# Performance work log

Hardware: AMD Instinct MI355X
Metric: run time of the kernel (lower is better)

The kernel has to match this reference:

```python
import jax, jax.numpy as jnp
import numpy as np

N_HEADS = 8
D_HEAD = 16
D_IN = 128
N_NODES = 50000
N_EDGES = 600000


def setup_inputs() -> dict:
    key = jax.random.key(0)
    ks = jax.random.split(key, 7)
    x = jax.random.normal(ks[0], (N_NODES, D_IN), dtype=jnp.float32)
    edge_attr = jax.random.normal(ks[1], (N_EDGES, D_IN), dtype=jnp.float32)
    edge_index = jax.random.randint(ks[2], (2, N_EDGES), 0, N_NODES, dtype=jnp.int32)
    # Linear weights stored as [in, out] so projection is x @ W.
    s = 1.0 / np.sqrt(D_IN)
    WQ = jax.random.normal(ks[3], (D_IN, N_HEADS * D_HEAD), dtype=jnp.float32) * s
    WK = jax.random.normal(ks[4], (D_IN, N_HEADS * D_HEAD), dtype=jnp.float32) * s
    WV = jax.random.normal(ks[5], (D_IN, N_HEADS * D_HEAD), dtype=jnp.float32) * s
    WE = jax.random.normal(ks[6], (D_IN, N_HEADS * D_HEAD), dtype=jnp.float32) * s
    return {"x": x, "edge_attr": edge_attr, "edge_index": edge_index,
            "WQ": WQ, "WK": WK, "WV": WV, "WE": WE}


def reference(x, edge_attr, edge_index, WQ, WK, WV, WE):
    N = x.shape[0]
    q = (x @ WQ).reshape(N, N_HEADS, D_HEAD)
    k = (x @ WK).reshape(N, N_HEADS, D_HEAD)
    v = (x @ WV).reshape(N, N_HEADS, D_HEAD)
    e_proj = (edge_attr @ WE).reshape(-1, N_HEADS, D_HEAD)
    row, col = edge_index[0], edge_index[1]
    # per-edge gather-compute: [E, H, D]
    alpha = (k[row] * q[col]) * (1.0 / np.sqrt(D_HEAD))
    alpha = jnp.clip(alpha, -5.0, 5.0) * e_proj
    e_out = alpha  # update_edge_feats=True
    alphax = jnp.exp(jnp.clip(alpha.sum(-1, keepdims=True), -5.0, 5.0))  # [E, H, 1]
    wV = jax.ops.segment_sum(v[row] * alphax, col, num_segments=N)  # [N, H, D]
    z = jax.ops.segment_sum(alphax, col, num_segments=N)            # [N, H, 1]
    h_out = wV / (z + 1e-6)
    return h_out, e_out
```

## Files before the change

### kernel.cpp

```cpp
#include <hip/hip_runtime.h>

#define DIN 128
#define NHEADS 8
#define DHEAD 16
#define NPB 32
#define EPB 64

typedef __attribute__((ext_vector_type(8))) short short8;
typedef __attribute__((ext_vector_type(4))) float f32x4;

__device__ __forceinline__ float clip5(float x) {
    return fminf(fmaxf(x, -5.0f), 5.0f);
}

__device__ __forceinline__ unsigned short f2bf(float f) {
    unsigned u = __float_as_uint(f);
    unsigned r = (u + 0x7FFF + ((u >> 16) & 1)) >> 16;
    return (unsigned short)r;
}

__device__ __forceinline__ float b2f(unsigned short u) {
    return __uint_as_float((unsigned)u << 16);
}

__device__ __forceinline__ float bflo(unsigned u) {
    return __uint_as_float(u << 16);
}
__device__ __forceinline__ float bfhi(unsigned u) {
    return __uint_as_float(u & 0xffff0000u);
}


__device__ __forceinline__ void tile_gemm(const float xs[][DIN], int r0, int cg,
                                          const float* __restrict__ W,
                                          float4 acc[4]) {
#pragma unroll 4
    for (int kk = 0; kk < DIN; kk += 4) {
        float4 a[4];
#pragma unroll
        for (int i = 0; i < 4; ++i)
            a[i] = *(const float4*)&xs[r0 + i][kk];
#pragma unroll
        for (int t = 0; t < 4; ++t) {
            float4 w = *(const float4*)&W[(kk + t) * DIN + (cg << 2)];
#pragma unroll
            for (int i = 0; i < 4; ++i) {
                float av = ((const float*)&a[i])[t];
                acc[i].x = fmaf(av, w.x, acc[i].x);
                acc[i].y = fmaf(av, w.y, acc[i].y);
                acc[i].z = fmaf(av, w.z, acc[i].z);
                acc[i].w = fmaf(av, w.w, acc[i].w);
            }
        }
    }
}

__global__ __launch_bounds__(256) void node_proj_kernel(
    const float* __restrict__ x, const float* __restrict__ WQ,
    const float* __restrict__ WK, const float* __restrict__ WV,
    unsigned short* __restrict__ qbf, unsigned short* __restrict__ kbf,
    unsigned short* __restrict__ vbf, int N) {
    __shared__ float xs[NPB][DIN];
    const int tid = threadIdx.x;
    const int n0 = blockIdx.x * NPB;

#pragma unroll
    for (int i = 0; i < NPB * DIN / (256 * 4); ++i) {
        int idx = (tid + i * 256) * 4;
        int r = idx / DIN, c = idx % DIN;
        float4 val = make_float4(0.f, 0.f, 0.f, 0.f);
        if (n0 + r < N) val = *(const float4*)&x[(long)(n0 + r) * DIN + c];
        *(float4*)&xs[r][c] = val;
    }
    __syncthreads();

    const int cg = tid & 31;
    const int ng = tid >> 5;
    const int r0 = ng * 4;

    const float* Ws[3] = {WQ, WK, WV};
    unsigned short* outs[3] = {qbf, kbf, vbf};
#pragma unroll
    for (int m = 0; m < 3; ++m) {
        float4 acc[4] = {make_float4(0,0,0,0), make_float4(0,0,0,0),
                         make_float4(0,0,0,0), make_float4(0,0,0,0)};
        tile_gemm(xs, r0, cg, Ws[m], acc);
#pragma unroll
        for (int i = 0; i < 4; ++i) {
            int n = n0 + r0 + i;
            if (n < N) {
                ushort4 b;
                b.x = f2bf(acc[i].x); b.y = f2bf(acc[i].y);
                b.z = f2bf(acc[i].z); b.w = f2bf(acc[i].w);
                *(ushort4*)&outs[m][(long)n * DIN + (cg << 2)] = b;
            }
        }
    }
}


__global__ __launch_bounds__(256) void degree_kernel(
    const int* __restrict__ cols, int* __restrict__ deg, int E) {
    int e = blockIdx.x * 256 + threadIdx.x;
    if (e < E) atomicAdd(&deg[cols[e]], 1);
}

__global__ __launch_bounds__(256) void block_sum_kernel(
    const int* __restrict__ deg, int* __restrict__ bsum, int N) {
    __shared__ int s[256];
    int tid = threadIdx.x;
    int i = blockIdx.x * 256 + tid;
    s[tid] = (i < N) ? deg[i] : 0;
    __syncthreads();
    for (int st = 128; st > 0; st >>= 1) {
        if (tid < st) s[tid] += s[tid + st];
        __syncthreads();
    }
    if (tid == 0) bsum[blockIdx.x] = s[0];
}

__global__ __launch_bounds__(256) void scan_bsum_kernel(int* __restrict__ bsum, int NB) {
    __shared__ int s[256];
    int tid = threadIdx.x;
    int v = (tid < NB) ? bsum[tid] : 0;
    s[tid] = v;
    __syncthreads();
    for (int off = 1; off < 256; off <<= 1) {
        int t = (tid >= off) ? s[tid - off] : 0;
        __syncthreads();
        s[tid] += t;
        __syncthreads();
    }
    if (tid < NB) bsum[tid] = s[tid] - v;
}

__global__ __launch_bounds__(256) void offsets_kernel(
    const int* __restrict__ deg, const int* __restrict__ bsumscan,
    int* __restrict__ offsets, int* __restrict__ cursor, int N, int E) {
    __shared__ int s[256];
    int tid = threadIdx.x;
    int i = blockIdx.x * 256 + tid;
    int v = (i < N) ? deg[i] : 0;
    s[tid] = v;
    __syncthreads();
    for (int off = 1; off < 256; off <<= 1) {
        int t = (tid >= off) ? s[tid - off] : 0;
        __syncthreads();
        s[tid] += t;
        __syncthreads();
    }
    int excl = s[tid] - v + bsumscan[blockIdx.x];
    if (i < N) { offsets[i] = excl; cursor[i] = excl; }
    if (blockIdx.x == 0 && tid == 0) offsets[N] = E;
}

__global__ __launch_bounds__(256) void scatter_kernel(
    const int* __restrict__ rows, const int* __restrict__ cols,
    int* __restrict__ cursor, int* __restrict__ elist,
    int* __restrict__ rows_s, int* __restrict__ cols_s, int E) {
    int e = blockIdx.x * 256 + threadIdx.x;
    if (e >= E) return;
    int c = cols[e];
    int pos = atomicAdd(&cursor[c], 1);
    elist[pos] = e;
    rows_s[pos] = rows[e];
    cols_s[pos] = c;
}


__global__ __launch_bounds__(256) void prep_wet_kernel(
    const float* __restrict__ WE, unsigned short* __restrict__ WEt) {
    int idx = blockIdx.x * 256 + threadIdx.x;
    int kk = idx >> 7, n = idx & 127;
    WEt[n * DIN + kk] = f2bf(WE[kk * DIN + n]);
}


__global__ __launch_bounds__(256) void edge_mfma_kernel(
    const float* __restrict__ edge_attr, const int* __restrict__ elist,
    const int* __restrict__ rows_s, const int* __restrict__ cols_s,
    const unsigned short* __restrict__ WEt, const unsigned short* __restrict__ qbf,
    const unsigned short* __restrict__ kbf, float* __restrict__ e_out,
    float* __restrict__ ax_s, int E) {
    const int tid = threadIdx.x;
    const int e0 = blockIdx.x * EPB;
    const int w = tid >> 6;
    const int l = tid & 63;
    const int lr = l & 15;
    const int lg = l >> 4;
    const int j = e0 + w * 16 + lr;
    const long eg = elist[j];
    const int er = rows_s[j];
    const int ec = cols_s[j];

    const float* arow = &edge_attr[eg * DIN + lg * 8];
    f32x4 ea[8];
#pragma unroll
    for (int ks = 0; ks < 4; ++ks) {
        ea[ks * 2]     = __builtin_nontemporal_load((const f32x4*)&arow[ks * 32]);
        ea[ks * 2 + 1] = __builtin_nontemporal_load((const f32x4*)&arow[ks * 32 + 4]);
    }
    const unsigned short* krow = &kbf[(long)er * DIN + lg * 4];
    const unsigned short* qrow = &qbf[(long)ec * DIN + lg * 4];
    ushort4 kv[8], qv[8];
#pragma unroll
    for (int ft = 0; ft < 8; ++ft) {
        kv[ft] = *(const ushort4*)&krow[ft * 16];
        qv[ft] = *(const ushort4*)&qrow[ft * 16];
    }
    __builtin_amdgcn_sched_barrier(0);

    short8 bfrag[4];
#pragma unroll
    for (int ks = 0; ks < 4; ++ks) {
        f32x4 a0 = ea[ks * 2], a1 = ea[ks * 2 + 1];
        short8 f;
        f[0] = (short)f2bf(a0[0]); f[1] = (short)f2bf(a0[1]);
        f[2] = (short)f2bf(a0[2]); f[3] = (short)f2bf(a0[3]);
        f[4] = (short)f2bf(a1[0]); f[5] = (short)f2bf(a1[1]);
        f[6] = (short)f2bf(a1[2]); f[7] = (short)f2bf(a1[3]);
        bfrag[ks] = f;
    }

#pragma unroll
    for (int ft = 0; ft < 8; ++ft) {
        f32x4 acc = (f32x4){0.f, 0.f, 0.f, 0.f};
#pragma unroll
        for (int ks = 0; ks < 4; ++ks) {
            short8 af = *(const short8*)&WEt[(ft * 16 + lr) * DIN + ks * 32 + lg * 8];
            acc = __builtin_amdgcn_mfma_f32_16x16x32_bf16(af, bfrag[ks], acc, 0, 0, 0);
        }
        const int f0 = ft * 16 + lg * 4;
        f32x4 t;
        t[0] = clip5(b2f(kv[ft].x) * b2f(qv[ft].x) * 0.25f) * acc[0];
        t[1] = clip5(b2f(kv[ft].y) * b2f(qv[ft].y) * 0.25f) * acc[1];
        t[2] = clip5(b2f(kv[ft].z) * b2f(qv[ft].z) * 0.25f) * acc[2];
        t[3] = clip5(b2f(kv[ft].w) * b2f(qv[ft].w) * 0.25f) * acc[3];
        __builtin_nontemporal_store(t, (f32x4*)&e_out[eg * DIN + f0]);

        float s = t[0] + t[1] + t[2] + t[3];
        s += __shfl_xor(s, 16);
        s += __shfl_xor(s, 32);
        float axv = __expf(clip5(s));
        if (lg == 0)
            ax_s[(long)j * NHEADS + ft] = axv;
    }
}


__global__ __launch_bounds__(256) void aggregate_kernel(
    const int* __restrict__ offsets, const int* __restrict__ rows_s,
    const float* __restrict__ ax_s, const unsigned short* __restrict__ vbf,
    float* __restrict__ h_out, int N) {
    int wid = blockIdx.x * 4 + (threadIdx.x >> 6);
    int lane = threadIdx.x & 63;
    if (wid >= N) return;
    int beg = offsets[wid], end = offsets[wid + 1];
    const int head = lane >> 3;

    float2 acc = make_float2(0.f, 0.f);
    float zacc = 0.f;

    for (int j = beg; j < end; j += 8) {
        int n = end - j; n = (n > 8) ? 8 : n;
        int r_[8]; float a_[8]; unsigned u_[8];
#pragma unroll
        for (int t = 0; t < 8; ++t)
            r_[t] = rows_s[j + ((t < n) ? t : 0)];
#pragma unroll
        for (int t = 0; t < 8; ++t) {
            a_[t] = (t < n) ? ax_s[(long)(j + t) * NHEADS + head] : 0.f;
            u_[t] = *(const unsigned*)&vbf[(long)r_[t] * DIN + lane * 2];
        }
#pragma unroll
        for (int t = 0; t < 8; ++t) {
            acc.x = fmaf(bflo(u_[t]), a_[t], acc.x);
            acc.y = fmaf(bfhi(u_[t]), a_[t], acc.y);
            zacc += a_[t];
        }
    }
    float inv = 1.0f / (zacc + 1e-6f);
    float2 res = make_float2(acc.x * inv, acc.y * inv);
    *(float2*)&h_out[(long)wid * DIN + lane * 2] = res;
}

extern "C" void kernel_launch(void* const* d_in, const int* in_sizes, int n_in,
                              void* d_out, int out_size, void* d_ws, size_t ws_size,
                              hipStream_t stream) {
    const float* x         = (const float*)d_in[0];
    const float* edge_attr = (const float*)d_in[1];
    const int*   edge_index= (const int*)d_in[2];
    const float* WQ        = (const float*)d_in[3];
    const float* WK        = (const float*)d_in[4];
    const float* WV        = (const float*)d_in[5];
    const float* WE        = (const float*)d_in[6];

    const int N = in_sizes[0] / DIN;
    const int E = in_sizes[2] / 2;
    const int NB = (N + 255) / 256;

    float* out   = (float*)d_out;
    float* h_out = out;
    float* e_out = out + (long)N * DIN;

    unsigned short* qbf = (unsigned short*)d_ws;
    unsigned short* kbf = qbf + (long)N * DIN;
    unsigned short* vbf = kbf + (long)N * DIN;
    float* ax_s = (float*)(vbf + (long)N * DIN);
    unsigned short* WEt = (unsigned short*)(ax_s + (long)E * NHEADS);
    int* ip      = (int*)(WEt + DIN * DIN);
    int* deg     = ip;
    int* cursor  = deg + N;
    int* offsets = cursor + N;
    int* bsum    = offsets + N + 1;
    int* elist   = bsum + 256;
    int* rows_s  = elist + E;
    int* cols_s  = rows_s + E;

    const int* rows = edge_index;
    const int* cols = edge_index + E;

    hipMemsetAsync(deg, 0, (size_t)N * sizeof(int), stream);

    node_proj_kernel<<<(N + NPB - 1) / NPB, 256, 0, stream>>>(x, WQ, WK, WV, qbf, kbf, vbf, N);
    prep_wet_kernel<<<DIN * DIN / 256, 256, 0, stream>>>(WE, WEt);

    degree_kernel<<<(E + 255) / 256, 256, 0, stream>>>(cols, deg, E);
    block_sum_kernel<<<NB, 256, 0, stream>>>(deg, bsum, N);
    scan_bsum_kernel<<<1, 256, 0, stream>>>(bsum, NB);
    offsets_kernel<<<NB, 256, 0, stream>>>(deg, bsum, offsets, cursor, N, E);
    scatter_kernel<<<(E + 255) / 256, 256, 0, stream>>>(rows, cols, cursor,
                                                        elist, rows_s, cols_s, E);

    edge_mfma_kernel<<<E / EPB, 256, 0, stream>>>(
        edge_attr, elist, rows_s, cols_s, WEt, qbf, kbf, e_out, ax_s, E);

    aggregate_kernel<<<(N + 3) / 4, 256, 0, stream>>>(
        offsets, rows_s, ax_s, vbf, h_out, N);
}
```

Before: 485.7 us.

## Fuse aggregation into edge kernel and move node projection to MFMA

```diff
diff --git a/kernel.cpp b/kernel.cpp
--- a/kernel.cpp
+++ b/kernel.cpp
@@ -3,7 +3,6 @@
 #define DIN 128
 #define NHEADS 8
 #define DHEAD 16
-#define NPB 32
 #define EPB 64
 
 typedef __attribute__((ext_vector_type(8))) short short8;
@@ -23,76 +22,68 @@
     return __uint_as_float((unsigned)u << 16);
 }
 
-__device__ __forceinline__ float bflo(unsigned u) {
-    return __uint_as_float(u << 16);
-}
-__device__ __forceinline__ float bfhi(unsigned u) {
-    return __uint_as_float(u & 0xffff0000u);
-}
-
-
-__device__ __forceinline__ void tile_gemm(const float xs[][DIN], int r0, int cg,
-                                          const float* __restrict__ W,
-                                          float4 acc[4]) {
-#pragma unroll 4
-    for (int kk = 0; kk < DIN; kk += 4) {
-        float4 a[4];
-#pragma unroll
-        for (int i = 0; i < 4; ++i)
-            a[i] = *(const float4*)&xs[r0 + i][kk];
-#pragma unroll
-        for (int t = 0; t < 4; ++t) {
-            float4 w = *(const float4*)&W[(kk + t) * DIN + (cg << 2)];
-#pragma unroll
-            for (int i = 0; i < 4; ++i) {
-                float av = ((const float*)&a[i])[t];
-                acc[i].x = fmaf(av, w.x, acc[i].x);
-                acc[i].y = fmaf(av, w.y, acc[i].y);
-                acc[i].z = fmaf(av, w.z, acc[i].z);
-                acc[i].w = fmaf(av, w.w, acc[i].w);
-            }
-        }
-    }
-}
-
-__global__ __launch_bounds__(256) void node_proj_kernel(
-    const float* __restrict__ x, const float* __restrict__ WQ,
-    const float* __restrict__ WK, const float* __restrict__ WV,
+
+__global__ __launch_bounds__(256) void prep_w_kernel(
+    const float* __restrict__ WQ, const float* __restrict__ WK,
+    const float* __restrict__ WV, const float* __restrict__ WE,
+    unsigned short* __restrict__ Wt) {
+    int idx = blockIdx.x * 256 + threadIdx.x;
+    int m = idx >> 14, r = idx & 16383;
+    int kk = r >> 7, n = r & 127;
+    const float* Ws[4] = {WQ, WK, WV, WE};
+    Wt[m * 16384 + n * DIN + kk] = f2bf(Ws[m][kk * DIN + n]);
+}
+
+
+__global__ __launch_bounds__(256) void node_mfma_kernel(
+    const float* __restrict__ x, const unsigned short* __restrict__ Wt,
     unsigned short* __restrict__ qbf, unsigned short* __restrict__ kbf,
     unsigned short* __restrict__ vbf, int N) {
-    __shared__ float xs[NPB][DIN];
     const int tid = threadIdx.x;
-    const int n0 = blockIdx.x * NPB;
-
-#pragma unroll
-    for (int i = 0; i < NPB * DIN / (256 * 4); ++i) {
-        int idx = (tid + i * 256) * 4;
-        int r = idx / DIN, c = idx % DIN;
-        float4 val = make_float4(0.f, 0.f, 0.f, 0.f);
-        if (n0 + r < N) val = *(const float4*)&x[(long)(n0 + r) * DIN + c];
-        *(float4*)&xs[r][c] = val;
-    }
-    __syncthreads();
-
-    const int cg = tid & 31;
-    const int ng = tid >> 5;
-    const int r0 = ng * 4;
-
-    const float* Ws[3] = {WQ, WK, WV};
+    const int w = tid >> 6;
+    const int l = tid & 63;
+    const int lr = l & 15;
+    const int lg = l >> 4;
+    int n = blockIdx.x * 64 + w * 16 + lr;
+    const bool ok = n < N;
+    const int nc = ok ? n : N - 1;
+
+    const float* xrow = &x[(long)nc * DIN + lg * 8];
+    f32x4 xa[8];
+#pragma unroll
+    for (int ks = 0; ks < 4; ++ks) {
+        xa[ks * 2]     = *(const f32x4*)&xrow[ks * 32];
+        xa[ks * 2 + 1] = *(const f32x4*)&xrow[ks * 32 + 4];
+    }
+    short8 bfrag[4];
+#pragma unroll
+    for (int ks = 0; ks < 4; ++ks) {
+        f32x4 a0 = xa[ks * 2], a1 = xa[ks * 2 + 1];
+        short8 f;
+        f[0] = (short)f2bf(a0[0]); f[1] = (short)f2bf(a0[1]);
+        f[2] = (short)f2bf(a0[2]); f[3] = (short)f2bf(a0[3]);
+        f[4] = (short)f2bf(a1[0]); f[5] = (short)f2bf(a1[1]);
+        f[6] = (short)f2bf(a1[2]); f[7] = (short)f2bf(a1[3]);
+        bfrag[ks] = f;
+    }
+
     unsigned short* outs[3] = {qbf, kbf, vbf};
 #pragma unroll
     for (int m = 0; m < 3; ++m) {
-        float4 acc[4] = {make_float4(0,0,0,0), make_float4(0,0,0,0),
-                         make_float4(0,0,0,0), make_float4(0,0,0,0)};
-        tile_gemm(xs, r0, cg, Ws[m], acc);
-#pragma unroll
-        for (int i = 0; i < 4; ++i) {
-            int n = n0 + r0 + i;
-            if (n < N) {
+        const unsigned short* Wm = Wt + m * 16384;
+#pragma unroll
+        for (int ft = 0; ft < 8; ++ft) {
+            f32x4 acc = (f32x4){0.f, 0.f, 0.f, 0.f};
+#pragma unroll
+            for (int ks = 0; ks < 4; ++ks) {
+                short8 af = *(const short8*)&Wm[(ft * 16 + lr) * DIN + ks * 32 + lg * 8];
+                acc = __builtin_amdgcn_mfma_f32_16x16x32_bf16(af, bfrag[ks], acc, 0, 0, 0);
+            }
+            if (ok) {
                 ushort4 b;
-                b.x = f2bf(acc[i].x); b.y = f2bf(acc[i].y);
-                b.z = f2bf(acc[i].z); b.w = f2bf(acc[i].w);
-                *(ushort4*)&outs[m][(long)n * DIN + (cg << 2)] = b;
+                b.x = f2bf(acc[0]); b.y = f2bf(acc[1]);
+                b.z = f2bf(acc[2]); b.w = f2bf(acc[3]);
+                *(ushort4*)&outs[m][(long)n * DIN + ft * 16 + lg * 4] = b;
             }
         }
     }
@@ -136,7 +127,7 @@
 
 __global__ __launch_bounds__(256) void offsets_kernel(
     const int* __restrict__ deg, const int* __restrict__ bsumscan,
-    int* __restrict__ offsets, int* __restrict__ cursor, int N, int E) {
+    int* __restrict__ cursor, int N) {
     __shared__ int s[256];
     int tid = threadIdx.x;
     int i = blockIdx.x * 256 + tid;
@@ -150,8 +141,7 @@
         __syncthreads();
     }
     int excl = s[tid] - v + bsumscan[blockIdx.x];
-    if (i < N) { offsets[i] = excl; cursor[i] = excl; }
-    if (blockIdx.x == 0 && tid == 0) offsets[N] = E;
+    if (i < N) cursor[i] = excl;
 }
 
 __global__ __launch_bounds__(256) void scatter_kernel(
@@ -168,20 +158,19 @@
 }
 
 
-__global__ __launch_bounds__(256) void prep_wet_kernel(
-    const float* __restrict__ WE, unsigned short* __restrict__ WEt) {
-    int idx = blockIdx.x * 256 + threadIdx.x;
-    int kk = idx >> 7, n = idx & 127;
-    WEt[n * DIN + kk] = f2bf(WE[kk * DIN + n]);
-}
-
-
-__global__ __launch_bounds__(256) void edge_mfma_kernel(
+__global__ __launch_bounds__(256) void edge_fused_kernel(
     const float* __restrict__ edge_attr, const int* __restrict__ elist,
     const int* __restrict__ rows_s, const int* __restrict__ cols_s,
     const unsigned short* __restrict__ WEt, const unsigned short* __restrict__ qbf,
-    const unsigned short* __restrict__ kbf, float* __restrict__ e_out,
-    float* __restrict__ ax_s, int E) {
+    const unsigned short* __restrict__ kbf, const unsigned short* __restrict__ vbf,
+    float* __restrict__ e_out, float* __restrict__ wV, float* __restrict__ z,
+    int E) {
+    __shared__ float wacc[EPB][DIN + 4];
+    __shared__ float zacc[EPB][NHEADS];
+    __shared__ int rank_s[EPB];
+    __shared__ int dest_s[EPB];
+    __shared__ int nranks_s;
+
     const int tid = threadIdx.x;
     const int e0 = blockIdx.x * EPB;
     const int w = tid >> 6;
@@ -189,6 +178,27 @@
     const int lr = l & 15;
     const int lg = l >> 4;
     const int j = e0 + w * 16 + lr;
+
+    for (int i = tid; i < EPB * (DIN + 4); i += 256)
+        ((float*)wacc)[i] = 0.f;
+    for (int i = tid; i < EPB * NHEADS; i += 256)
+        ((float*)zacc)[i] = 0.f;
+
+    if (tid < EPB) {
+        int c = cols_s[e0 + tid];
+        int cp = (tid == 0) ? -1 : cols_s[e0 + tid - 1];
+        int b = (c != cp) ? 1 : 0;
+        int s = b;
+#pragma unroll
+        for (int off = 1; off < EPB; off <<= 1) {
+            int t = __shfl_up(s, off);
+            if (tid >= off) s += t;
+        }
+        rank_s[tid] = s - 1;
+        if (b) dest_s[s - 1] = c;
+        if (tid == EPB - 1) nranks_s = s;
+    }
+
     const long eg = elist[j];
     const int er = rows_s[j];
     const int ec = cols_s[j];
@@ -202,11 +212,13 @@
     }
     const unsigned short* krow = &kbf[(long)er * DIN + lg * 4];
     const unsigned short* qrow = &qbf[(long)ec * DIN + lg * 4];
-    ushort4 kv[8], qv[8];
+    const unsigned short* vrow = &vbf[(long)er * DIN + lg * 4];
+    ushort4 kv[8], qv[8], vv[8];
 #pragma unroll
     for (int ft = 0; ft < 8; ++ft) {
         kv[ft] = *(const ushort4*)&krow[ft * 16];
         qv[ft] = *(const ushort4*)&qrow[ft * 16];
+        vv[ft] = *(const ushort4*)&vrow[ft * 16];
     }
     __builtin_amdgcn_sched_barrier(0);
 
@@ -222,6 +234,9 @@
         bfrag[ks] = f;
     }
 
+    __syncthreads();
+    const int myrank = rank_s[w * 16 + lr];
+
 #pragma unroll
     for (int ft = 0; ft < 8; ++ft) {
         f32x4 acc = (f32x4){0.f, 0.f, 0.f, 0.f};
@@ -242,46 +257,44 @@
         s += __shfl_xor(s, 16);
         s += __shfl_xor(s, 32);
         float axv = __expf(clip5(s));
-        if (lg == 0)
-            ax_s[(long)j * NHEADS + ft] = axv;
-    }
-}
-
-
-__global__ __launch_bounds__(256) void aggregate_kernel(
-    const int* __restrict__ offsets, const int* __restrict__ rows_s,
-    const float* __restrict__ ax_s, const unsigned short* __restrict__ vbf,
-    float* __restrict__ h_out, int N) {
-    int wid = blockIdx.x * 4 + (threadIdx.x >> 6);
-    int lane = threadIdx.x & 63;
-    if (wid >= N) return;
-    int beg = offsets[wid], end = offsets[wid + 1];
-    const int head = lane >> 3;
-
-    float2 acc = make_float2(0.f, 0.f);
-    float zacc = 0.f;
-
-    for (int j = beg; j < end; j += 8) {
-        int n = end - j; n = (n > 8) ? 8 : n;
-        int r_[8]; float a_[8]; unsigned u_[8];
-#pragma unroll
-        for (int t = 0; t < 8; ++t)
-            r_[t] = rows_s[j + ((t < n) ? t : 0)];
-#pragma unroll
-        for (int t = 0; t < 8; ++t) {
-            a_[t] = (t < n) ? ax_s[(long)(j + t) * NHEADS + head] : 0.f;
-            u_[t] = *(const unsigned*)&vbf[(long)r_[t] * DIN + lane * 2];
-        }
-#pragma unroll
-        for (int t = 0; t < 8; ++t) {
-            acc.x = fmaf(bflo(u_[t]), a_[t], acc.x);
-            acc.y = fmaf(bfhi(u_[t]), a_[t], acc.y);
-            zacc += a_[t];
-        }
-    }
-    float inv = 1.0f / (zacc + 1e-6f);
-    float2 res = make_float2(acc.x * inv, acc.y * inv);
-    *(float2*)&h_out[(long)wid * DIN + lane * 2] = res;
+
+        atomicAdd(&wacc[myrank][f0 + 0], axv * b2f(vv[ft].x));
+        atomicAdd(&wacc[myrank][f0 + 1], axv * b2f(vv[ft].y));
+        atomicAdd(&wacc[myrank][f0 + 2], axv * b2f(vv[ft].z));
+        atomicAdd(&wacc[myrank][f0 + 3], axv * b2f(vv[ft].w));
+        if (lg == 0) atomicAdd(&zacc[myrank][ft], axv);
+    }
+
+    __syncthreads();
+    const int nr = nranks_s;
+    for (int base = 0; base < nr; base += 2) {
+        int r = base + (tid >> 7);
+        int f = tid & 127;
+        if (r < nr) {
+            float val = wacc[r][f];
+            if (val != 0.f) atomicAdd(&wV[(long)dest_s[r] * DIN + f], val);
+        }
+    }
+    if (tid < EPB * NHEADS) {
+        int r = tid >> 3, h = tid & 7;
+        if (r < nr) {
+            float val = zacc[r][h];
+            if (val != 0.f) atomicAdd(&z[(long)dest_s[r] * NHEADS + h], val);
+        }
+    }
+}
+
+
+__global__ __launch_bounds__(256) void normalize_kernel(
+    float* __restrict__ h, const float* __restrict__ z, int N) {
+    long idx = (long)blockIdx.x * 256 + threadIdx.x;
+    if (idx >= (long)N * 32) return;
+    int n = (int)(idx >> 5);
+    int fq = (int)(idx & 31);
+    float inv = 1.0f / (z[n * NHEADS + (fq >> 2)] + 1e-6f);
+    f32x4 v = *(f32x4*)&h[(long)n * DIN + fq * 4];
+    v[0] *= inv; v[1] *= inv; v[2] *= inv; v[3] *= inv;
+    *(f32x4*)&h[(long)n * DIN + fq * 4] = v;
 }
 
 extern "C" void kernel_launch(void* const* d_in, const int* in_sizes, int n_in,
@@ -306,13 +319,12 @@
     unsigned short* qbf = (unsigned short*)d_ws;
     unsigned short* kbf = qbf + (long)N * DIN;
     unsigned short* vbf = kbf + (long)N * DIN;
-    float* ax_s = (float*)(vbf + (long)N * DIN);
-    unsigned short* WEt = (unsigned short*)(ax_s + (long)E * NHEADS);
-    int* ip      = (int*)(WEt + DIN * DIN);
+    float* z = (float*)(vbf + (long)N * DIN);
+    unsigned short* Wt = (unsigned short*)(z + (long)N * NHEADS);
+    int* ip      = (int*)(Wt + 4 * 16384);
     int* deg     = ip;
     int* cursor  = deg + N;
-    int* offsets = cursor + N;
-    int* bsum    = offsets + N + 1;
+    int* bsum    = cursor + N;
     int* elist   = bsum + 256;
     int* rows_s  = elist + E;
     int* cols_s  = rows_s + E;
@@ -321,20 +333,22 @@
     const int* cols = edge_index + E;
 
     hipMemsetAsync(deg, 0, (size_t)N * sizeof(int), stream);
-
-    node_proj_kernel<<<(N + NPB - 1) / NPB, 256, 0, stream>>>(x, WQ, WK, WV, qbf, kbf, vbf, N);
-    prep_wet_kernel<<<DIN * DIN / 256, 256, 0, stream>>>(WE, WEt);
+    hipMemsetAsync(z, 0, (size_t)N * NHEADS * sizeof(float), stream);
+    hipMemsetAsync(h_out, 0, (size_t)N * DIN * sizeof(float), stream);
+
+    prep_w_kernel<<<4 * 16384 / 256, 256, 0, stream>>>(WQ, WK, WV, WE, Wt);
+    node_mfma_kernel<<<(N + 63) / 64, 256, 0, stream>>>(x, Wt, qbf, kbf, vbf, N);
 
     degree_kernel<<<(E + 255) / 256, 256, 0, stream>>>(cols, deg, E);
     block_sum_kernel<<<NB, 256, 0, stream>>>(deg, bsum, N);
     scan_bsum_kernel<<<1, 256, 0, stream>>>(bsum, NB);
-    offsets_kernel<<<NB, 256, 0, stream>>>(deg, bsum, offsets, cursor, N, E);
+    offsets_kernel<<<NB, 256, 0, stream>>>(deg, bsum, cursor, N);
     scatter_kernel<<<(E + 255) / 256, 256, 0, stream>>>(rows, cols, cursor,
                                                         elist, rows_s, cols_s, E);
 
-    edge_mfma_kernel<<<E / EPB, 256, 0, stream>>>(
-        edge_attr, elist, rows_s, cols_s, WEt, qbf, kbf, e_out, ax_s, E);
-
-    aggregate_kernel<<<(N + 3) / 4, 256, 0, stream>>>(
-        offsets, rows_s, ax_s, vbf, h_out, N);
-}
+    edge_fused_kernel<<<E / EPB, 256, 0, stream>>>(
+        edge_attr, elist, rows_s, cols_s, Wt + 3 * 16384, qbf, kbf, vbf,
+        e_out, h_out, z, E);
+
+    normalize_kernel<<<(int)(((long)N * 32 + 255) / 256), 256, 0, stream>>>(h_out, z, N);
+}
```

Result: slower. 757.5 us (+56.0%).
